# Optimization experiments

Measured on AMD Instinct MI355X. Metric: run time of the kernel, lower is better.

Reference implementation:

```python
import jax, jax.numpy as jnp
import numpy as np

N_HEADS = 4
HEAD_DIM = 64
NEG_SLOPE = 0.2
TIME_PE_DIM = 16


def time_pe(date):
    # TimePositionalEncoding: sin/cos features; 8 sin + 8 cos == pe_dim (16), no projection needed
    t = date.astype(jnp.float32) / 10000.0
    div = jnp.exp(jnp.arange(0, TIME_PE_DIM, 2, dtype=jnp.float32) * (-jnp.log(10000.0) / TIME_PE_DIM))
    arg = t[:, None] * div[None, :]  # [N, 8]
    return jnp.concatenate([jnp.sin(arg), jnp.cos(arg)], axis=-1)  # [N, 16]


def pearl_pe(x, edge_index, Wp, bp):
    # PEARL positional embedding approximated as mean-neighbor aggregation over the
    # union of all relations followed by a learned linear + tanh -> [N, 32]
    N = x.shape[0]
    src = edge_index[:, 0, :].reshape(-1)
    dst = edge_index[:, 1, :].reshape(-1)
    agg = jax.ops.segment_sum(x[src], dst, num_segments=N)
    deg = jax.ops.segment_sum(jnp.ones_like(dst, jnp.float32), dst, num_segments=N)
    agg = agg / jnp.maximum(deg, 1.0)[:, None]
    return jnp.tanh(agg @ Wp + bp)


def gatv2(x, src, dst, Wl, Wr, att, b):
    # GATv2 message passing for one edge type; dropout is identity (eval mode)
    N = x.shape[0]
    xl = (x @ Wl).reshape(N, N_HEADS, HEAD_DIM)
    xr = (x @ Wr).reshape(N, N_HEADS, HEAD_DIM)
    m = xl[src] + xr[dst]                                   # [E, H, C]
    e = jnp.sum(jax.nn.leaky_relu(m, NEG_SLOPE) * att, -1)  # [E, H]
    emax = jax.ops.segment_max(e, dst, num_segments=N)
    emax = jnp.where(jnp.isfinite(emax), emax, 0.0)
    ex = jnp.exp(e - emax[dst])
    denom = jax.ops.segment_sum(ex, dst, num_segments=N)
    alpha = ex / (denom[dst] + 1e-16)                       # segment softmax over in-edges
    out = jax.ops.segment_sum(xl[src] * alpha[..., None], dst, num_segments=N)
    return out.reshape(N, N_HEADS * HEAD_DIM) + b


def rel_agg(h_rel, W, b, a):
    # attention-weighted combination across relation outputs: h_rel [N, R, hidden]
    s = jnp.einsum('nrh,h->nr', jnp.tanh(h_rel @ W + b), a)
    w = jax.nn.softmax(s, axis=-1)
    return jnp.einsum('nr,nrh->nh', w, h_rel)


def gnn_layer(h, edge_index, Wl, Wr, att, b, aW, ab, aa):
    R = edge_index.shape[0]
    # HeteroConv aggr='sum': sum GATv2 outputs across the 5 relations
    conv_sum = gatv2(h, edge_index[0, 0], edge_index[0, 1], Wl[0], Wr[0], att[0], b[0])
    for r in range(1, R):
        conv_sum = conv_sum + gatv2(h, edge_index[r, 0], edge_index[r, 1], Wl[r], Wr[r], att[r], b[r])
    # original forward feeds conv_output['stock'] for every relation key (identical copies)
    h_rel = jnp.broadcast_to(conv_sum[:, None, :], (conv_sum.shape[0], R, conv_sum.shape[1]))
    h = rel_agg(h_rel, aW, ab, aa)
    return jax.nn.relu(h)  # dropout identity in eval


def reference(x, date_tensor, edge_index, pearl_W, pearl_b, Wl0, Wr0, att0, b0,
              Wl1, Wr1, att1, b1, aggW, aggb, agga, out_W1, out_b1, out_W2, out_b2):
    pe = pearl_pe(x, edge_index, pearl_W, pearl_b)          # [N, 32]
    tpe = time_pe(date_tensor)                              # [N, 16]
    h = jnp.concatenate([x, pe, tpe], axis=1)               # [N, 112]
    h = gnn_layer(h, edge_index, Wl0, Wr0, att0, b0, aggW[0], aggb[0], agga[0])
    h = gnn_layer(h, edge_index, Wl1, Wr1, att1, b1, aggW[1], aggb[1], agga[1])
    h = jax.nn.relu(h @ out_W1 + out_b1)
    return h @ out_W2 + out_b2                              # [N, 3]


def setup_inputs():
    key = jax.random.key(0)
    ks = jax.random.split(key, 20)
    N, E, R = 20000, 320000, 5
    IN, PE, HID = 64, 32, 256
    IN0 = IN + PE + TIME_PE_DIM  # 112

    def nrm(k, shp, sc=0.05):
        return jax.random.normal(k, shp, jnp.float32) * sc

    return {
        'x': jax.random.normal(ks[0], (N, IN), jnp.float32),
        'date_tensor': jax.random.randint(ks[1], (N,), 0, 20000, jnp.int32),
        'edge_index': jax.random.randint(ks[2], (R, 2, E), 0, N, jnp.int32),
        'pearl_W': nrm(ks[3], (IN, PE)),
        'pearl_b': jnp.zeros((PE,), jnp.float32),
        'Wl0': nrm(ks[4], (R, IN0, HID)),
        'Wr0': nrm(ks[5], (R, IN0, HID)),
        'att0': nrm(ks[6], (R, N_HEADS, HEAD_DIM)),
        'b0': jnp.zeros((R, HID), jnp.float32),
        'Wl1': nrm(ks[7], (R, HID, HID)),
        'Wr1': nrm(ks[8], (R, HID, HID)),
        'att1': nrm(ks[9], (R, N_HEADS, HEAD_DIM)),
        'b1': jnp.zeros((R, HID), jnp.float32),
        'aggW': nrm(ks[10], (2, HID, HID)),
        'aggb': jnp.zeros((2, HID), jnp.float32),
        'agga': nrm(ks[11], (2, HID)),
        'out_W1': nrm(ks[12], (HID, HID // 2)),
        'out_b1': jnp.zeros((HID // 2,), jnp.float32),
        'out_W2': nrm(ks[13], (HID // 2, 3)),
        'out_b2': jnp.zeros((3,), jnp.float32),
    }
```

## Files before the change

### kernel.cpp

```cpp
#include <hip/hip_runtime.h>
#include <math.h>

typedef __bf16 bf16x8 __attribute__((ext_vector_type(8)));
typedef __bf16 bf16x4 __attribute__((ext_vector_type(4)));
typedef float f32x4 __attribute__((ext_vector_type(4)));
typedef unsigned short u16x8 __attribute__((ext_vector_type(8)));

#define GLD16(src, dst)                                                        \
    __builtin_amdgcn_global_load_lds(                                          \
        (const __attribute__((address_space(1))) void*)(src),                  \
        (__attribute__((address_space(3))) void*)(dst), 16, 0, 0)

__device__ inline float bf2f(unsigned short u) {
    union { unsigned int i; float f; } c;
    c.i = ((unsigned int)u) << 16;
    return c.f;
}


__global__ __launch_bounds__(256) void count_kernel(const int* __restrict__ ei,
                                                    int* __restrict__ cnt, int N, int E) {
    int idx = blockIdx.x * 256 + threadIdx.x;
    if (idx >= 5 * E) return;
    int r = idx / E;
    int e = idx - r * E;
    int dst = ei[(size_t)r * 2 * E + E + e];
    atomicAdd(&cnt[r * N + dst], 1);
}

__global__ __launch_bounds__(256) void scanA_kernel(const int* __restrict__ cnt,
                                                    int* __restrict__ off,
                                                    int* __restrict__ csums, int N, int NC) {
    int r = blockIdx.y, c = blockIdx.x, t = threadIdx.x;
    int idx0 = c * 1024 + t * 4;
    int v0 = (idx0 + 0 < N) ? cnt[r * N + idx0 + 0] : 0;
    int v1 = (idx0 + 1 < N) ? cnt[r * N + idx0 + 1] : 0;
    int v2 = (idx0 + 2 < N) ? cnt[r * N + idx0 + 2] : 0;
    int v3 = (idx0 + 3 < N) ? cnt[r * N + idx0 + 3] : 0;
    int ts = v0 + v1 + v2 + v3;
    __shared__ int sd[256];
    sd[t] = ts;
    __syncthreads();
    for (int s = 1; s < 256; s <<= 1) {
        int add = (t >= s) ? sd[t - s] : 0;
        __syncthreads();
        sd[t] += add;
        __syncthreads();
    }
    int excl = sd[t] - ts;
    size_t base = (size_t)r * (N + 1);
    if (idx0 + 0 < N) off[base + idx0 + 0] = excl;
    if (idx0 + 1 < N) off[base + idx0 + 1] = excl + v0;
    if (idx0 + 2 < N) off[base + idx0 + 2] = excl + v0 + v1;
    if (idx0 + 3 < N) off[base + idx0 + 3] = excl + v0 + v1 + v2;
    if (t == 255) csums[r * NC + c] = sd[255];
}

__global__ __launch_bounds__(64) void scanB_kernel(int* __restrict__ csums,
                                                   int* __restrict__ off, int N, int NC) {
    int r = threadIdx.x;
    if (r < 5) {
        int run = 0;
        for (int c = 0; c < NC; c++) {
            int t = csums[r * NC + c];
            csums[r * NC + c] = run;
            run += t;
        }
        off[(size_t)r * (N + 1) + N] = run;
    }
}

__global__ __launch_bounds__(256) void scanC_kernel(int* __restrict__ off,
                                                    const int* __restrict__ csums,
                                                    int* __restrict__ cur,
                                                    int N, int NC) {
    int r = blockIdx.y, c = blockIdx.x, t = threadIdx.x;
    int add = csums[r * NC + c];
    int idx0 = c * 1024 + t * 4;
    size_t base = (size_t)r * (N + 1);
#pragma unroll
    for (int j = 0; j < 4; j++)
        if (idx0 + j < N) {
            int v = off[base + idx0 + j] + add;
            off[base + idx0 + j] = v;
            cur[r * N + idx0 + j] = v;
        }
}

__global__ __launch_bounds__(256) void scatter_kernel(const int* __restrict__ ei,
                                                      int* __restrict__ cur,
                                                      unsigned short* __restrict__ srcs,
                                                      int N, int E) {
    int idx = blockIdx.x * 256 + threadIdx.x;
    if (idx >= 5 * E) return;
    int r = idx / E;
    int e = idx - r * E;
    int src = ei[(size_t)r * 2 * E + e];
    int dst = ei[(size_t)r * 2 * E + E + e];
    int pos = atomicAdd(&cur[r * N + dst], 1);
    srcs[(size_t)r * E + pos] = (unsigned short)src;
}


__global__ __launch_bounds__(256) void xcvt_kernel(const float* __restrict__ x,
                                                   unsigned short* __restrict__ xb, int total) {
    int idx = (blockIdx.x * 256 + threadIdx.x) * 4;
    if (idx >= total) return;
    float4 v = *(const float4*)(x + idx);
    __bf16 b0 = (__bf16)v.x, b1 = (__bf16)v.y, b2 = (__bf16)v.z, b3 = (__bf16)v.w;
    unsigned short* p = xb + idx;
    p[0] = *(unsigned short*)&b0;
    p[1] = *(unsigned short*)&b1;
    p[2] = *(unsigned short*)&b2;
    p[3] = *(unsigned short*)&b3;
}


__global__ __launch_bounds__(256) void pearl_h0_kernel(
    const float* __restrict__ x, const unsigned short* __restrict__ xb,
    const int* __restrict__ date,
    const int* __restrict__ off, const unsigned short* __restrict__ srcs,
    const float* __restrict__ pW, const float* __restrict__ pb,
    float* __restrict__ h0, int N, int E) {
    int lane = threadIdx.x & 63;
    int wid = blockIdx.x * 4 + (threadIdx.x >> 6);
    if (wid >= N) return;
    int n = __builtin_amdgcn_readfirstlane(wid);

    float acc = 0.f;
    int deg = 0;
    for (int r = 0; r < 5; r++) {
        int kb = off[(size_t)r * (N + 1) + n];
        int ke = off[(size_t)r * (N + 1) + n + 1];
        deg += ke - kb;
        const unsigned short* sp = srcs + (size_t)r * E;
        int k = kb;
        for (; k + 16 <= ke; k += 16) {
            int ix[16];
#pragma unroll
            for (int j = 0; j < 16; j++) ix[j] = sp[k + j];
            float a[16];
#pragma unroll
            for (int j = 0; j < 16; j++) a[j] = bf2f(xb[(size_t)ix[j] * 64 + lane]);
            float s0 = ((a[0] + a[1]) + (a[2] + a[3])) + ((a[4] + a[5]) + (a[6] + a[7]));
            float s1 = ((a[8] + a[9]) + (a[10] + a[11])) + ((a[12] + a[13]) + (a[14] + a[15]));
            acc += s0 + s1;
        }
        for (; k + 4 <= ke; k += 4) {
            int i0 = sp[k], i1 = sp[k + 1], i2 = sp[k + 2], i3 = sp[k + 3];
            float a0 = bf2f(xb[(size_t)i0 * 64 + lane]);
            float a1 = bf2f(xb[(size_t)i1 * 64 + lane]);
            float a2 = bf2f(xb[(size_t)i2 * 64 + lane]);
            float a3 = bf2f(xb[(size_t)i3 * 64 + lane]);
            acc += (a0 + a1) + (a2 + a3);
        }
        for (; k < ke; k++) acc += bf2f(xb[(size_t)sp[k] * 64 + lane]);
    }
    float an = acc / fmaxf((float)deg, 1.0f);

    float s = (lane < 32) ? pb[lane] : 0.f;
#pragma unroll 8
    for (int c = 0; c < 64; c++) {
        float av = __shfl(an, c, 64);
        if (lane < 32) s = fmaf(av, pW[c * 32 + lane], s);
    }

    h0[(size_t)n * 112 + lane] = x[(size_t)n * 64 + lane];
    if (lane < 32) h0[(size_t)n * 112 + 64 + lane] = tanhf(s);
    if (lane < 16) {
        float t = (float)date[n] / 10000.0f;
        int i = lane & 7;
        float dv = expf((float)(2 * i) * (-0.57564627324851148f));
        float arg = t * dv;
        h0[(size_t)n * 112 + 96 + lane] = (lane < 8) ? sinf(arg) : cosf(arg);
    }
}


__global__ __launch_bounds__(256) void pack_a_kernel(
    const float* __restrict__ A, __bf16* __restrict__ Ah, __bf16* __restrict__ Al,
    int M, int K, int Mp, int KT) {
    int KG = KT * 4;
    int idx = blockIdx.x * 256 + threadIdx.x;
    if (idx >= Mp * KG) return;
    int m = idx / KG, kgg = idx - m * KG;
    int kt = kgg >> 2, kg = kgg & 3;
    int k0 = kt * 32 + kg * 8;
    int mt = m >> 4, mr = m & 15;
    size_t out = (((size_t)mt * KT + kt) * 64 + kg * 16 + mr) * 8;
    bf16x8 hv, lv;
#pragma unroll
    for (int j = 0; j < 8; j++) {
        int k = k0 + j;
        float v = (m < M && k < K) ? A[(size_t)m * K + k] : 0.f;
        __bf16 h = (__bf16)v;
        hv[j] = h;
        lv[j] = (__bf16)(v - (float)h);
    }
    *(bf16x8*)(Ah + out) = hv;
    *(bf16x8*)(Al + out) = lv;
}


__global__ __launch_bounds__(256) void pack_w_kernel(
    const float* __restrict__ Wl0, const float* __restrict__ Wr0,
    const float* __restrict__ Wl1, const float* __restrict__ Wr1,
    const float* __restrict__ W1,
    __bf16* __restrict__ Wph, __bf16* __restrict__ Wpl) {
    const int S0 = 32768, S1 = 65536;
    int t = blockIdx.y;
    const float* W;
    int K, Nc, KT;
    size_t dst;
    if (t < 5)       { W = Wl0 + (size_t)t * 112 * 256;        K = 112; Nc = 256; KT = 4; dst = (size_t)t * S0; }
    else if (t < 10) { W = Wr0 + (size_t)(t - 5) * 112 * 256;  K = 112; Nc = 256; KT = 4; dst = 163840 + (size_t)(t - 5) * S0; }
    else if (t < 15) { W = Wl1 + (size_t)(t - 10) * 256 * 256; K = 256; Nc = 256; KT = 8; dst = 327680 + (size_t)(t - 10) * S1; }
    else if (t < 20) { W = Wr1 + (size_t)(t - 15) * 256 * 256; K = 256; Nc = 256; KT = 8; dst = 655360 + (size_t)(t - 15) * S1; }
    else             { W = W1;                                  K = 256; Nc = 128; KT = 8; dst = 983040; }
    int entries = (Nc / 16) * KT * 64;
    int idx = blockIdx.x * 256 + threadIdx.x;
    if (idx >= entries) return;
    int nt = idx / (KT * 64);
    int rem = idx - nt * (KT * 64);
    int kt = rem >> 6, lane = rem & 63;
    int kg = lane >> 4, nr = lane & 15;
    bf16x8 hv, lv;
#pragma unroll
    for (int j = 0; j < 8; j++) {
        int k = kt * 32 + kg * 8 + j;
        float v = (k < K) ? W[(size_t)k * Nc + nt * 16 + nr] : 0.f;
        __bf16 h = (__bf16)v;
        hv[j] = h;
        lv[j] = (__bf16)(v - (float)h);
    }
    *(bf16x8*)(Wph + dst + (size_t)idx * 8) = hv;
    *(bf16x8*)(Wpl + dst + (size_t)idx * 8) = lv;
}


__global__ __launch_bounds__(256) void gemm_mfma(
    const __bf16* __restrict__ Ah, const __bf16* __restrict__ Al,
    const __bf16* __restrict__ WLh, const __bf16* __restrict__ WLl,
    const __bf16* __restrict__ WRh, const __bf16* __restrict__ WRl,
    size_t strideB, void* __restrict__ Cl, void* __restrict__ Cr, size_t CstrideBytes,
    int M, int Nout, int KT, const float* __restrict__ bias, int do_relu,
    int npL, int npR, int out_bf16, int NYT, int per_bx) {
    int lin = blockIdx.x;
    int bx = lin / per_bx, rem = lin % per_bx;
    int by = rem % NYT; rem /= NYT;
    int side = rem & 1;
    int r = rem >> 1;

    const __bf16* Bh = (side ? WRh : WLh) + (size_t)r * strideB;
    const __bf16* Bl = (side ? WRl : WLl) + (size_t)r * strideB;
    char* C = (char*)(side ? Cr : Cl) + (size_t)r * CstrideBytes;
    int np = side ? npR : npL;

    __shared__ __bf16 sAh[8 * 512], sAl[8 * 512], sBh[8 * 512], sBl[8 * 512];

    int tid = threadIdx.x, lane = tid & 63, w = tid >> 6;
    int wr = w >> 1, wc = w & 1;

    f32x4 acc[4][4] = {};

    for (int kt = 0; kt < KT; ++kt) {
        int tl = w * 2;
        size_t a0 = ((size_t)(bx * 8 + tl) * KT + kt) * 512 + lane * 8;
        size_t a1 = ((size_t)(bx * 8 + tl + 1) * KT + kt) * 512 + lane * 8;
        size_t b0 = ((size_t)(by * 8 + tl) * KT + kt) * 512 + lane * 8;
        size_t b1 = ((size_t)(by * 8 + tl + 1) * KT + kt) * 512 + lane * 8;
        GLD16(Ah + a0, sAh + tl * 512);
        GLD16(Ah + a1, sAh + (tl + 1) * 512);
        GLD16(Bh + b0, sBh + tl * 512);
        GLD16(Bh + b1, sBh + (tl + 1) * 512);
        if (np >= 2) {
            GLD16(Al + a0, sAl + tl * 512);
            GLD16(Al + a1, sAl + (tl + 1) * 512);
        }
        if (np == 3) {
            GLD16(Bl + b0, sBl + tl * 512);
            GLD16(Bl + b1, sBl + (tl + 1) * 512);
        }
        __syncthreads();

        bf16x8 ah[4], al[4], bh[4], bl[4];
#pragma unroll
        for (int i = 0; i < 4; i++) {
            ah[i] = *(const bf16x8*)(sAh + (wr * 4 + i) * 512 + lane * 8);
            bh[i] = *(const bf16x8*)(sBh + (wc * 4 + i) * 512 + lane * 8);
        }
        if (np >= 2) {
#pragma unroll
            for (int i = 0; i < 4; i++)
                al[i] = *(const bf16x8*)(sAl + (wr * 4 + i) * 512 + lane * 8);
        }
        if (np == 3) {
#pragma unroll
            for (int i = 0; i < 4; i++)
                bl[i] = *(const bf16x8*)(sBl + (wc * 4 + i) * 512 + lane * 8);
        }
#pragma unroll
        for (int i = 0; i < 4; i++)
#pragma unroll
            for (int j = 0; j < 4; j++) {
                acc[i][j] = __builtin_amdgcn_mfma_f32_16x16x32_bf16(ah[i], bh[j], acc[i][j], 0, 0, 0);
                if (np >= 2)
                    acc[i][j] = __builtin_amdgcn_mfma_f32_16x16x32_bf16(al[i], bh[j], acc[i][j], 0, 0, 0);
                if (np == 3)
                    acc[i][j] = __builtin_amdgcn_mfma_f32_16x16x32_bf16(ah[i], bl[j], acc[i][j], 0, 0, 0);
            }
        __syncthreads();
    }

    int rb = bx * 128 + wr * 64, cb = by * 128 + wc * 64;
#pragma unroll
    for (int i = 0; i < 4; i++) {
#pragma unroll
        for (int j = 0; j < 4; j++) {
            int row0 = rb + i * 16 + (lane >> 4) * 4;
            int col = cb + j * 16 + (lane & 15);
            float bv = bias ? bias[col] : 0.f;
#pragma unroll
            for (int q = 0; q < 4; q++) {
                int row = row0 + q;
                if (row < M) {
                    float v = acc[i][j][q] + bv;
                    if (do_relu) v = fmaxf(v, 0.f);
                    if (out_bf16)
                        ((__bf16*)C)[(size_t)row * Nout + col] = (__bf16)v;
                    else
                        ((float*)C)[(size_t)row * Nout + col] = v;
                }
            }
        }
    }
}


__global__ __launch_bounds__(256) void gat5_kernel(
    const unsigned short* __restrict__ xl5, const unsigned short* __restrict__ xr5,
    const float* __restrict__ att,
    const int* __restrict__ csrOff,
    const unsigned short* __restrict__ csrSrc,
    __bf16* __restrict__ Ah, __bf16* __restrict__ Al,
    const float* __restrict__ bvec,
    int N, int E) {
    int lane = threadIdx.x & 63;
    int wid = blockIdx.x * 4 + (threadIdx.x >> 6);
    if (wid >= N) return;
    int n = __builtin_amdgcn_readfirstlane(wid);
    int e = lane >> 4;
    int sub = lane & 15;
    int cb = (sub >> 2) * 64 + (sub & 3) * 16;
    int wc = cb + e * 4;

    float4 cv = {0.f, 0.f, 0.f, 0.f};
#pragma unroll
    for (int r = 0; r < 5; r++) {
        float4 b = *(const float4*)(bvec + r * 256 + wc);
        cv.x += b.x; cv.y += b.y; cv.z += b.z; cv.w += b.w;
    }

    for (int r = 0; r < 5; r++) {
        const unsigned short* xl = xl5 + (size_t)r * N * 256;
        float rv[16], av[16];
        {
            const unsigned short* xrp = xr5 + ((size_t)r * N + n) * 256 + cb;
            u16x8 q0 = *(const u16x8*)(xrp);
            u16x8 q1 = *(const u16x8*)(xrp + 8);
#pragma unroll
            for (int j = 0; j < 8; j++) { rv[j] = bf2f(q0[j]); rv[8 + j] = bf2f(q1[j]); }
#pragma unroll
            for (int j = 0; j < 16; j += 4) {
                float4 a = *(const float4*)(att + r * 256 + cb + j);
                av[j] = a.x; av[j + 1] = a.y; av[j + 2] = a.z; av[j + 3] = a.w;
            }
        }

        float m = -3.0e38f, d = 0.f;
        float A[16];
#pragma unroll
        for (int j = 0; j < 16; j++) A[j] = 0.f;

        const int* off = csrOff + (size_t)r * (N + 1);
        const unsigned short* sp = csrSrc + (size_t)r * E;
        int kb = off[n], ke = off[n + 1];
        if (kb < ke) {
            int kl = ke - 1;
            int ki = kb + e;
            int s = sp[(ki <= kl) ? ki : kl];
            float c[16];
            {
                const unsigned short* xp = xl + (size_t)s * 256 + cb;
                u16x8 q0 = *(const u16x8*)(xp);
                u16x8 q1 = *(const u16x8*)(xp + 8);
#pragma unroll
                for (int j = 0; j < 8; j++) { c[j] = bf2f(q0[j]); c[8 + j] = bf2f(q1[j]); }
            }
            for (int k = kb; k < ke; k += 4) {
                int kn = k + 4 + e;
                int sn = sp[(kn <= kl) ? kn : kl];
                const unsigned short* np_ = xl + (size_t)sn * 256 + cb;
                u16x8 n0 = *(const u16x8*)(np_);
                u16x8 n1 = *(const u16x8*)(np_ + 8);

                float p = 0.f;
#pragma unroll
                for (int j = 0; j < 16; j++) {
                    float t = c[j] + rv[j];
                    t = (t > 0.f) ? t : 0.2f * t;
                    p = fmaf(t, av[j], p);
                }
                p += __shfl_xor(p, 1, 64);
                p += __shfl_xor(p, 2, 64);
                bool valid = (k + e) < ke;
                if (!valid) p = -3.0e38f;

                if (__any(p > m)) {
                    float nm = fmaxf(m, p);
                    float sc = __expf(m - nm);
                    d *= sc;
#pragma unroll
                    for (int j = 0; j < 16; j++) A[j] *= sc;
                    m = nm;
                }
                float wg = valid ? __expf(p - m) : 0.f;
                d += wg;
#pragma unroll
                for (int j = 0; j < 16; j++) A[j] = fmaf(wg, c[j], A[j]);

#pragma unroll
                for (int j = 0; j < 8; j++) { c[j] = bf2f(n0[j]); c[8 + j] = bf2f(n1[j]); }
            }
        }

        float M = fmaxf(m, __shfl_xor(m, 16, 64));
        M = fmaxf(M, __shfl_xor(M, 32, 64));
        float sc = __expf(m - M);
        d *= sc;
        d += __shfl_xor(d, 16, 64);
        d += __shfl_xor(d, 32, 64);
#pragma unroll
        for (int j = 0; j < 16; j++) {
            A[j] *= sc;
            A[j] += __shfl_xor(A[j], 16, 64);
            A[j] += __shfl_xor(A[j], 32, 64);
        }

        float inv = 1.0f / (d + 1e-16f);
        cv.x = fmaf(A[e * 4 + 0], inv, cv.x);
        cv.y = fmaf(A[e * 4 + 1], inv, cv.y);
        cv.z = fmaf(A[e * 4 + 2], inv, cv.z);
        cv.w = fmaf(A[e * 4 + 3], inv, cv.w);
    }

    cv.x = fmaxf(cv.x, 0.f);
    cv.y = fmaxf(cv.y, 0.f);
    cv.z = fmaxf(cv.z, 0.f);
    cv.w = fmaxf(cv.w, 0.f);
    float vv[4] = {cv.x, cv.y, cv.z, cv.w};
    bf16x4 hv, lv;
#pragma unroll
    for (int j = 0; j < 4; j++) {
        __bf16 h = (__bf16)vv[j];
        hv[j] = h;
        lv[j] = (__bf16)(vv[j] - (float)h);
    }
    size_t outp = (((size_t)(n >> 4) * 8 + (wc >> 5)) * 64 + ((wc >> 3) & 3) * 16 + (n & 15)) * 8 + (wc & 7);
    *(bf16x4*)(Ah + outp) = hv;
    *(bf16x4*)(Al + outp) = lv;
}


__global__ __launch_bounds__(256) void head_kernel(const float* __restrict__ hm,
                                                   const float* __restrict__ W2,
                                                   const float* __restrict__ b2,
                                                   float* __restrict__ out, int N) {
    int lane = threadIdx.x & 63;
    int wid = blockIdx.x * 4 + (threadIdx.x >> 6);
    if (wid >= N) return;
    int n = __builtin_amdgcn_readfirstlane(wid);
    float a0 = hm[(size_t)n * 128 + lane];
    float a1 = hm[(size_t)n * 128 + 64 + lane];
    float s0 = a0 * W2[lane * 3 + 0] + a1 * W2[(64 + lane) * 3 + 0];
    float s1 = a0 * W2[lane * 3 + 1] + a1 * W2[(64 + lane) * 3 + 1];
    float s2 = a0 * W2[lane * 3 + 2] + a1 * W2[(64 + lane) * 3 + 2];
#pragma unroll
    for (int sft = 1; sft < 64; sft <<= 1) {
        s0 += __shfl_xor(s0, sft, 64);
        s1 += __shfl_xor(s1, sft, 64);
        s2 += __shfl_xor(s2, sft, 64);
    }
    if (lane == 0) {
        out[(size_t)n * 3 + 0] = s0 + b2[0];
        out[(size_t)n * 3 + 1] = s1 + b2[1];
        out[(size_t)n * 3 + 2] = s2 + b2[2];
    }
}


extern "C" void kernel_launch(void* const* d_in, const int* in_sizes, int n_in,
                              void* d_out, int out_size, void* d_ws, size_t ws_size,
                              hipStream_t stream) {
    const float* x    = (const float*)d_in[0];
    const int* date   = (const int*)d_in[1];
    const int* ei     = (const int*)d_in[2];
    const float* pW   = (const float*)d_in[3];
    const float* pb   = (const float*)d_in[4];
    const float* Wl0  = (const float*)d_in[5];
    const float* Wr0  = (const float*)d_in[6];
    const float* att0 = (const float*)d_in[7];
    const float* b0   = (const float*)d_in[8];
    const float* Wl1  = (const float*)d_in[9];
    const float* Wr1  = (const float*)d_in[10];
    const float* att1 = (const float*)d_in[11];
    const float* b1   = (const float*)d_in[12];
    const float* outW1 = (const float*)d_in[16];
    const float* outb1 = (const float*)d_in[17];
    const float* outW2 = (const float*)d_in[18];
    const float* outb2 = (const float*)d_in[19];
    float* out = (float*)d_out;

    int N = in_sizes[0] / 64;
    int E = in_sizes[2] / 10;
    int Mp = ((N + 127) / 128) * 128;
    int MT = Mp / 128;
    int NC = (N + 1023) / 1024;

    char* ws = (char*)d_ws;
    size_t o = 0;
    auto alloc = [&](size_t bytes) -> char* {
        char* p = ws + o;
        o += (bytes + 255) & ~(size_t)255;
        return p;
    };
    int* cur               = (int*)alloc((size_t)5 * N * 4);
    int* csrOff            = (int*)alloc((size_t)5 * (N + 1) * 4);
    unsigned short* csrSrc = (unsigned short*)alloc((size_t)5 * E * 2);
    int* csums             = (int*)alloc((size_t)5 * NC * 4);
    unsigned short* xb16   = (unsigned short*)alloc((size_t)N * 64 * 2);
    float* h0              = (float*)alloc((size_t)N * 112 * 4);
    unsigned short* xl5    = (unsigned short*)alloc((size_t)5 * N * 256 * 2);
    unsigned short* xr5    = (unsigned short*)alloc((size_t)5 * N * 256 * 2);
    __bf16* Aph            = (__bf16*)alloc((size_t)Mp * 256 * 2);
    __bf16* Apl            = (__bf16*)alloc((size_t)Mp * 256 * 2);
    __bf16* Wph            = (__bf16*)alloc((size_t)1015808 * 2);
    __bf16* Wpl            = (__bf16*)alloc((size_t)1015808 * 2);
    float* hmid            = (float*)xl5;
    (void)ws_size;

    const size_t S0 = 32768, S1 = 65536;
    const size_t oWl0 = 0, oWr0 = 163840, oWl1 = 327680, oWr1 = 655360, oW1 = 983040;
    size_t xstride = (size_t)N * 256 * 2;

    int totE = 5 * E;

    hipMemsetAsync(cur, 0, (size_t)5 * N * 4, stream);
    count_kernel<<<(totE + 255) / 256, 256, 0, stream>>>(ei, cur, N, E);
    scanA_kernel<<<dim3(NC, 5), 256, 0, stream>>>(cur, csrOff, csums, N, NC);
    scanB_kernel<<<1, 64, 0, stream>>>(csums, csrOff, N, NC);
    scanC_kernel<<<dim3(NC, 5), 256, 0, stream>>>(csrOff, csums, cur, N, NC);
    scatter_kernel<<<(totE + 255) / 256, 256, 0, stream>>>(ei, cur, csrSrc, N, E);

    xcvt_kernel<<<(N * 64 / 4 + 255) / 256, 256, 0, stream>>>(x, xb16, N * 64);
    pearl_h0_kernel<<<(N + 3) / 4, 256, 0, stream>>>(x, xb16, date, csrOff, csrSrc, pW, pb, h0, N, E);

    pack_w_kernel<<<dim3(32, 21, 1), 256, 0, stream>>>(Wl0, Wr0, Wl1, Wr1, outW1, Wph, Wpl);

    pack_a_kernel<<<(Mp * 16 + 255) / 256, 256, 0, stream>>>(h0, Aph, Apl, N, 112, Mp, 4);
    gemm_mfma<<<MT * 20, 256, 0, stream>>>(
        Aph, Apl, Wph + oWl0, Wpl + oWl0, Wph + oWr0, Wpl + oWr0, S0,
        xl5, xr5, xstride, N, 256, 4, nullptr, 0, 2, 1, 1, 2, 20);
    gat5_kernel<<<(N + 3) / 4, 256, 0, stream>>>(xl5, xr5, att0, csrOff, csrSrc,
                                                 Aph, Apl, b0, N, E);

    gemm_mfma<<<MT * 20, 256, 0, stream>>>(
        Aph, Apl, Wph + oWl1, Wpl + oWl1, Wph + oWr1, Wpl + oWr1, S1,
        xl5, xr5, xstride, N, 256, 8, nullptr, 0, 2, 1, 1, 2, 20);
    gat5_kernel<<<(N + 3) / 4, 256, 0, stream>>>(xl5, xr5, att1, csrOff, csrSrc,
                                                 Aph, Apl, b1, N, E);

    gemm_mfma<<<MT, 256, 0, stream>>>(
        Aph, Apl, Wph + oW1, Wpl + oW1, Wph + oW1, Wpl + oW1, 0,
        hmid, hmid, 0, N, 128, 8, outb1, 1, 3, 3, 0, 1, 1);
    head_kernel<<<(N + 3) / 4, 256, 0, stream>>>(hmid, outW2, outb2, out, N);
}
```

Baseline: 755.5 us.

## Vectorize PEARL gather, regroup GEMM block order, enlarge GAT blocks

The PEARL aggregation now has each half-wave handle alternate neighbours, loading two bf16 values per lane as a 32-bit word, then combining the halves with a cross-lane shuffle. This halves the number of gather instructions per edge. The GEMM block index mapping is reordered so that groups of 8 row tiles walk the same weight panel together, with a bounds check for padded tiles, which is meant to improve L2 reuse of the B panels. gat5 now runs 512-thread blocks with 8 nodes each, where before it ran 256-thread blocks with 4.

```diff
diff --git a/kernel.cpp b/kernel.cpp
--- a/kernel.cpp
+++ b/kernel.cpp
@@ -126,8 +126,10 @@
     int wid = blockIdx.x * 4 + (threadIdx.x >> 6);
     if (wid >= N) return;
     int n = __builtin_amdgcn_readfirstlane(wid);
-
-    float acc = 0.f;
+    int pr = lane >> 5;
+    int c2 = (lane & 31) * 2;
+
+    float a0 = 0.f, a1 = 0.f;
     int deg = 0;
     for (int r = 0; r < 5; r++) {
         int kb = off[(size_t)r * (N + 1) + n];
@@ -136,33 +138,43 @@
         const unsigned short* sp = srcs + (size_t)r * E;
         int k = kb;
         for (; k + 16 <= ke; k += 16) {
-            int ix[16];
-#pragma unroll
-            for (int j = 0; j < 16; j++) ix[j] = sp[k + j];
-            float a[16];
-#pragma unroll
-            for (int j = 0; j < 16; j++) a[j] = bf2f(xb[(size_t)ix[j] * 64 + lane]);
-            float s0 = ((a[0] + a[1]) + (a[2] + a[3])) + ((a[4] + a[5]) + (a[6] + a[7]));
-            float s1 = ((a[8] + a[9]) + (a[10] + a[11])) + ((a[12] + a[13]) + (a[14] + a[15]));
-            acc += s0 + s1;
-        }
-        for (; k + 4 <= ke; k += 4) {
-            int i0 = sp[k], i1 = sp[k + 1], i2 = sp[k + 2], i3 = sp[k + 3];
-            float a0 = bf2f(xb[(size_t)i0 * 64 + lane]);
-            float a1 = bf2f(xb[(size_t)i1 * 64 + lane]);
-            float a2 = bf2f(xb[(size_t)i2 * 64 + lane]);
-            float a3 = bf2f(xb[(size_t)i3 * 64 + lane]);
-            acc += (a0 + a1) + (a2 + a3);
-        }
-        for (; k < ke; k++) acc += bf2f(xb[(size_t)sp[k] * 64 + lane]);
-    }
-    float an = acc / fmaxf((float)deg, 1.0f);
+            unsigned int u[8];
+#pragma unroll
+            for (int j = 0; j < 8; j++) {
+                int row = sp[k + 2 * j + pr];
+                u[j] = *(const unsigned int*)(xb + (size_t)row * 64 + c2);
+            }
+#pragma unroll
+            for (int j = 0; j < 8; j++) {
+                a0 += bf2f((unsigned short)(u[j] & 0xffff));
+                a1 += bf2f((unsigned short)(u[j] >> 16));
+            }
+        }
+        for (; k + 2 <= ke; k += 2) {
+            int row = sp[k + pr];
+            unsigned int u = *(const unsigned int*)(xb + (size_t)row * 64 + c2);
+            a0 += bf2f((unsigned short)(u & 0xffff));
+            a1 += bf2f((unsigned short)(u >> 16));
+        }
+        if (k < ke) {
+            int row = sp[k];
+            unsigned int u = *(const unsigned int*)(xb + (size_t)row * 64 + c2);
+            if (pr == 0) {
+                a0 += bf2f((unsigned short)(u & 0xffff));
+                a1 += bf2f((unsigned short)(u >> 16));
+            }
+        }
+    }
+    a0 += __shfl_xor(a0, 32, 64);
+    a1 += __shfl_xor(a1, 32, 64);
+    float dn = fmaxf((float)deg, 1.0f);
+    float an0 = a0 / dn, an1 = a1 / dn;
 
     float s = (lane < 32) ? pb[lane] : 0.f;
-#pragma unroll 8
-    for (int c = 0; c < 64; c++) {
-        float av = __shfl(an, c, 64);
-        if (lane < 32) s = fmaf(av, pW[c * 32 + lane], s);
+#pragma unroll
+    for (int cc = 0; cc < 64; cc++) {
+        float av = __shfl((cc & 1) ? an1 : an0, cc >> 1, 64);
+        if (lane < 32) s = fmaf(av, pW[cc * 32 + lane], s);
     }
 
     h0[(size_t)n * 112 + lane] = x[(size_t)n * 64 + lane];
@@ -244,12 +256,16 @@
     const __bf16* __restrict__ WRh, const __bf16* __restrict__ WRl,
     size_t strideB, void* __restrict__ Cl, void* __restrict__ Cr, size_t CstrideBytes,
     int M, int Nout, int KT, const float* __restrict__ bias, int do_relu,
-    int npL, int npR, int out_bf16, int NYT, int per_bx) {
-    int lin = blockIdx.x;
-    int bx = lin / per_bx, rem = lin % per_bx;
-    int by = rem % NYT; rem /= NYT;
-    int side = rem & 1;
-    int r = rem >> 1;
+    int npL, int npR, int out_bf16, int NYT, int MTp, int NPANEL) {
+    int p = blockIdx.x;
+    int stride = 8 * NPANEL;
+    int g = p / stride, rem = p % stride;
+    int slot = rem % 8, panel = rem / 8;
+    int bx = g * 8 + slot;
+    if (bx >= MTp) return;
+    int by = panel % NYT;
+    int side = (panel / NYT) & 1;
+    int r = panel / (NYT * 2);
 
     const __bf16* Bh = (side ? WRh : WLh) + (size_t)r * strideB;
     const __bf16* Bl = (side ? WRl : WLl) + (size_t)r * strideB;
@@ -337,7 +353,7 @@
 }
 
 
-__global__ __launch_bounds__(256) void gat5_kernel(
+__global__ __launch_bounds__(512) void gat5_kernel(
     const unsigned short* __restrict__ xl5, const unsigned short* __restrict__ xr5,
     const float* __restrict__ att,
     const int* __restrict__ csrOff,
@@ -346,7 +362,7 @@
     const float* __restrict__ bvec,
     int N, int E) {
     int lane = threadIdx.x & 63;
-    int wid = blockIdx.x * 4 + (threadIdx.x >> 6);
+    int wid = blockIdx.x * 8 + (threadIdx.x >> 6);
     if (wid >= N) return;
     int n = __builtin_amdgcn_readfirstlane(wid);
     int e = lane >> 4;
@@ -525,6 +541,7 @@
     int E = in_sizes[2] / 10;
     int Mp = ((N + 127) / 128) * 128;
     int MT = Mp / 128;
+    int MT8 = (MT + 7) / 8;
     int NC = (N + 1023) / 1024;
 
     char* ws = (char*)d_ws;
@@ -568,20 +585,20 @@
     pack_w_kernel<<<dim3(32, 21, 1), 256, 0, stream>>>(Wl0, Wr0, Wl1, Wr1, outW1, Wph, Wpl);
 
     pack_a_kernel<<<(Mp * 16 + 255) / 256, 256, 0, stream>>>(h0, Aph, Apl, N, 112, Mp, 4);
-    gemm_mfma<<<MT * 20, 256, 0, stream>>>(
+    gemm_mfma<<<MT8 * 8 * 20, 256, 0, stream>>>(
         Aph, Apl, Wph + oWl0, Wpl + oWl0, Wph + oWr0, Wpl + oWr0, S0,
-        xl5, xr5, xstride, N, 256, 4, nullptr, 0, 2, 1, 1, 2, 20);
-    gat5_kernel<<<(N + 3) / 4, 256, 0, stream>>>(xl5, xr5, att0, csrOff, csrSrc,
+        xl5, xr5, xstride, N, 256, 4, nullptr, 0, 2, 1, 1, 2, MT, 20);
+    gat5_kernel<<<(N + 7) / 8, 512, 0, stream>>>(xl5, xr5, att0, csrOff, csrSrc,
                                                  Aph, Apl, b0, N, E);
 
-    gemm_mfma<<<MT * 20, 256, 0, stream>>>(
+    gemm_mfma<<<MT8 * 8 * 20, 256, 0, stream>>>(
         Aph, Apl, Wph + oWl1, Wpl + oWl1, Wph + oWr1, Wpl + oWr1, S1,
-        xl5, xr5, xstride, N, 256, 8, nullptr, 0, 2, 1, 1, 2, 20);
-    gat5_kernel<<<(N + 3) / 4, 256, 0, stream>>>(xl5, xr5, att1, csrOff, csrSrc,
+        xl5, xr5, xstride, N, 256, 8, nullptr, 0, 2, 1, 1, 2, MT, 20);
+    gat5_kernel<<<(N + 7) / 8, 512, 0, stream>>>(xl5, xr5, att1, csrOff, csrSrc,
                                                  Aph, Apl, b1, N, E);
 
-    gemm_mfma<<<MT, 256, 0, stream>>>(
+    gemm_mfma<<<MT8 * 8, 256, 0, stream>>>(
         Aph, Apl, Wph + oW1, Wpl + oW1, Wph + oW1, Wpl + oW1, 0,
-        hmid, hmid, 0, N, 128, 8, outb1, 1, 3, 3, 0, 1, 1);
+        hmid, hmid, 0, N, 128, 8, outb1, 1, 3, 3, 0, 1, MT, 1);
     head_kernel<<<(N + 3) / 4, 256, 0, stream>>>(hmid, outW2, outb2, out, N);
 }
```

New measurement: 762.7 us. No clear change (+0.9%).
